# Optimization experiments

Measured on AMD Instinct MI355X. Metric: run time of the kernel, lower is better.

The kernel has to match this reference:

```python
import jax, jax.numpy as jnp
import numpy as np

EMBED_DIM = 512
NUM_HEADS = 8
HEAD_DIM = EMBED_DIM // NUM_HEADS
EDGE_DIM = 16
B, N = 2, 2048


def setup_inputs() -> dict:
    key = jax.random.key(0)
    ks = jax.random.split(key, 16)
    s = 1.0 / np.sqrt(EMBED_DIM)
    inp = {
        "x": jax.random.normal(ks[0], (B, N, EMBED_DIM), dtype=jnp.float32),
        "adjacency": jax.random.uniform(ks[1], (B, N, N), dtype=jnp.float32),
        # torch.nn.Linear stores weight as (out, in); we keep that convention
        "Wq": jax.random.uniform(ks[2], (EMBED_DIM, EMBED_DIM), minval=-s, maxval=s),
        "bq": jax.random.uniform(ks[3], (EMBED_DIM,), minval=-s, maxval=s),
        "Wk": jax.random.uniform(ks[4], (EMBED_DIM, EMBED_DIM), minval=-s, maxval=s),
        "bk": jax.random.uniform(ks[5], (EMBED_DIM,), minval=-s, maxval=s),
        "Wv": jax.random.uniform(ks[6], (EMBED_DIM, EMBED_DIM), minval=-s, maxval=s),
        "bv": jax.random.uniform(ks[7], (EMBED_DIM,), minval=-s, maxval=s),
        "Wo": jax.random.uniform(ks[8], (EMBED_DIM, EMBED_DIM), minval=-s, maxval=s),
        "bo": jax.random.uniform(ks[9], (EMBED_DIM,), minval=-s, maxval=s),
        # edge MLP: Linear(1 -> edge_dim) then Linear(edge_dim -> num_heads)
        "We1": jax.random.uniform(ks[10], (EDGE_DIM, 1), minval=-1.0, maxval=1.0),
        "be1": jax.random.uniform(ks[11], (EDGE_DIM,), minval=-1.0, maxval=1.0),
        "We2": jax.random.uniform(ks[12], (NUM_HEADS, EDGE_DIM), minval=-0.25, maxval=0.25),
        "be2": jax.random.uniform(ks[13], (NUM_HEADS,), minval=-0.25, maxval=0.25),
        "edge_bias": jnp.zeros((NUM_HEADS,), dtype=jnp.float32),
    }
    return inp


def reference(x, adjacency, Wq, bq, Wk, bk, Wv, bv, Wo, bo, We1, be1, We2, be2, edge_bias):
    b, n, _ = x.shape
    scale = HEAD_DIM ** (-0.5)

    def split_heads(t):  # (b, n, E) -> (b, H, n, d)
        return t.reshape(b, n, NUM_HEADS, HEAD_DIM).transpose(0, 2, 1, 3)

    q = split_heads(x @ Wq.T + bq)
    k = split_heads(x @ Wk.T + bk)
    v = split_heads(x @ Wv.T + bv)

    # (b, H, n, n)
    attn_scores = jnp.einsum('bhid,bhjd->bhij', q, k) * scale

    # edge MLP applied pointwise to each adjacency entry: 1 -> edge_dim -> num_heads
    # hidden: (b, n, n, edge_dim)
    hidden = jax.nn.relu(adjacency[..., None] * We1[:, 0] + be1)
    edge_attn = jnp.einsum('bijE,hE->bhij', hidden, We2) + be2[None, :, None, None]

    boost = adjacency[:, None, :, :] * edge_bias[None, :, None, None]
    attn_scores = attn_scores + edge_attn + boost

    attn_probs = jax.nn.softmax(attn_scores, axis=-1)
    out = jnp.einsum('bhij,bhjd->bhid', attn_probs, v)
    out = out.transpose(0, 2, 1, 3).reshape(b, n, EMBED_DIM)
    out = out @ Wo.T + bo
    return out
```

## Files before the change

kernel.cpp:

```cpp
#include <hip/hip_runtime.h>
#include <stdint.h>


#define SEQ 2048
#define EMB 512
#define NH  8
#define HD  64
#define NB  2
#define L2E 1.4426950408889634f

typedef unsigned int   u32;
typedef unsigned short u16;
typedef u32   u32x4  __attribute__((ext_vector_type(4)));
typedef float f32x4  __attribute__((ext_vector_type(4)));
typedef __bf16 bf16x8 __attribute__((ext_vector_type(8)));

#define MFMA16(a, b, c) __builtin_amdgcn_mfma_f32_16x16x32_bf16((a), (b), (c), 0, 0, 0)

static __device__ __forceinline__ u16 f2bf(float f) {
  return __builtin_bit_cast(u16, (__bf16)f);
}
static __device__ __forceinline__ bf16x8 ldfrag(const u16* p) {
  return __builtin_bit_cast(bf16x8, *(const u32x4*)p);
}

__global__ void prep_kernel(const float* __restrict__ x,
                            const float* __restrict__ Wq, const float* __restrict__ Wk,
                            const float* __restrict__ Wv, const float* __restrict__ Wo,
                            const float* __restrict__ We1, const float* __restrict__ be1,
                            const float* __restrict__ We2, const float* __restrict__ be2,
                            const float* __restrict__ ebias,
                            u16* __restrict__ xb, u16* __restrict__ wqkv,
                            u16* __restrict__ wob, float* __restrict__ co) {
  const int blk = blockIdx.x, tid = threadIdx.x;
  if (blk < 2048) {
    int i = (blk * 256 + tid) * 4;
    float4 v = *(const float4*)(x + i);
    u32 lo = (u32)f2bf(v.x) | ((u32)f2bf(v.y) << 16);
    u32 hi = (u32)f2bf(v.z) | ((u32)f2bf(v.w) << 16);
    *(uint2*)(xb + i) = make_uint2(lo, hi);
  } else if (blk < 3072) {
    int i = ((blk - 2048) * 256 + tid) * 4;
    int m = i >> 18;
    int off = i & 262143;
    const float* src = (m == 0) ? Wq : ((m == 1) ? Wk : ((m == 2) ? Wv : Wo));
    u16* dst = (m < 3) ? (wqkv + (size_t)m * 262144) : wob;
    float4 v = *(const float4*)(src + off);
    u32 lo = (u32)f2bf(v.x) | ((u32)f2bf(v.y) << 16);
    u32 hi = (u32)f2bf(v.z) | ((u32)f2bf(v.w) << 16);
    *(uint2*)(dst + off) = make_uint2(lo, hi);
  } else {
    const int e = tid & 15, h = tid >> 4;
    if (tid < 128) {
      co[49 + e * 8 + h] = 0.0f;
      if (h == 0) { co[17 + e] = 0.0f; co[33 + e] = 0.0f; }
    }
    __syncthreads();
    if (tid < 128) {
      float w1 = We1[e], b1 = be1[e], w2 = We2[h * 16 + e];
      float u0 = b1, u1 = w1 + b1;
      bool on  = (u0 >= 0.0f) && (u1 >= 0.0f);
      bool off = (u0 <= 0.0f) && (u1 <= 0.0f);
      bool crossing = (!on) && (!off);
      float ca = on ? (w2 * b1) : (crossing ? 0.5f * w2 * b1 : 0.0f);
      float cb = on ? (w2 * w1) : (crossing ? 0.5f * w2 * w1 : 0.0f);
      #pragma unroll
      for (int d = 1; d < 16; d <<= 1) { ca += __shfl_xor(ca, d); cb += __shfl_xor(cb, d); }
      if (e == 0) { co[h] = (be2[h] + ca) * L2E; co[8 + h] = (ebias[h] + cb) * L2E; }
      unsigned long long msk = __ballot(crossing);
      int midx = __popcll(msk & 0xFFFFull & ((1ull << e) - 1ull));
      int mcnt = __popcll(msk & 0xFFFFull);
      if (crossing) {
        co[49 + midx * 8 + h] = 0.5f * w2 * L2E;
        if (h == 0) { co[17 + midx] = w1; co[33 + midx] = b1; }
      }
      if (tid == 0) ((int*)co)[16] = mcnt;
    }
  }
}

#define LDA 40
__global__ __launch_bounds__(256) void gemm_qkv_kernel(
    const u16* __restrict__ A, const u16* __restrict__ Bm,
    const float* __restrict__ bq, const float* __restrict__ bk, const float* __restrict__ bv,
    u16* __restrict__ qh, u16* __restrict__ kh, u16* __restrict__ vh)
{
  __shared__ u16 As[64 * LDA];
  __shared__ u16 Bs[128 * LDA];
  const int tid = threadIdx.x;
  const int lane = tid & 63, w = tid >> 6;
  const int q = lane >> 4, l15 = lane & 15;
  const int m0 = blockIdx.y * 64;
  const int n0 = blockIdx.x * 128;

  f32x4 acc[4][2];
  f32x4 zero = {0.f, 0.f, 0.f, 0.f};
  #pragma unroll
  for (int i = 0; i < 4; i++) { acc[i][0] = zero; acc[i][1] = zero; }

  const bool isA = tid < 128;
  const int arow = tid >> 1, ahalf = tid & 1;
  const int brow = tid - 128;
  const u16* ga = A  + (size_t)(m0 + arow) * EMB + ahalf * 16;
  const u16* gb = Bm + (size_t)(n0 + brow) * EMB;
  u16* la = &As[arow * LDA + ahalf * 16];
  u16* lb = &Bs[brow * LDA];

  u32x4 p0, p1, p2, p3;
  if (isA) {
    p0 = *(const u32x4*)(ga); p1 = *(const u32x4*)(ga + 8); ga += 32;
  } else {
    p0 = *(const u32x4*)(gb);      p1 = *(const u32x4*)(gb + 8);
    p2 = *(const u32x4*)(gb + 16); p3 = *(const u32x4*)(gb + 24); gb += 32;
  }

  for (int k0 = 0; k0 < EMB; k0 += 32) {
    __syncthreads();
    if (isA) { *(u32x4*)(la) = p0; *(u32x4*)(la + 8) = p1; }
    else {
      *(u32x4*)(lb)      = p0; *(u32x4*)(lb + 8)  = p1;
      *(u32x4*)(lb + 16) = p2; *(u32x4*)(lb + 24) = p3;
    }
    __syncthreads();
    if (k0 + 32 < EMB) {
      if (isA) { p0 = *(const u32x4*)(ga); p1 = *(const u32x4*)(ga + 8); ga += 32; }
      else {
        p0 = *(const u32x4*)(gb);      p1 = *(const u32x4*)(gb + 8);
        p2 = *(const u32x4*)(gb + 16); p3 = *(const u32x4*)(gb + 24); gb += 32;
      }
    }
    bf16x8 af[4], bfr[2];
    #pragma unroll
    for (int mi = 0; mi < 4; mi++)
      af[mi] = ldfrag(&As[(mi*16 + l15) * LDA + q*8]);
    #pragma unroll
    for (int ni = 0; ni < 2; ni++)
      bfr[ni] = ldfrag(&Bs[(w*32 + ni*16 + l15) * LDA + q*8]);
    #pragma unroll
    for (int mi = 0; mi < 4; mi++)
      #pragma unroll
      for (int ni = 0; ni < 2; ni++)
        acc[mi][ni] = MFMA16(af[mi], bfr[ni], acc[mi][ni]);
  }

  const int mat = n0 >> 9;
  const float* bias = (mat == 0) ? bq : ((mat == 1) ? bk : bv);
  u16* dst = (mat == 0) ? qh : ((mat == 1) ? kh : vh);
  const float mul = (mat == 0) ? 0.125f * L2E : 1.0f;

  #pragma unroll
  for (int mi = 0; mi < 4; mi++) {
    int rowb = m0 + mi*16 + q*4;
    #pragma unroll
    for (int ni = 0; ni < 2; ni++) {
      int col = n0 + w*32 + ni*16 + l15;
      int oo = col & 511;
      float bsv = bias[oo];
      int hh = oo >> 6, dd = oo & 63;
      #pragma unroll
      for (int r = 0; r < 4; r++) {
        int grow = rowb + r;
        int b_ = grow >> 11, n_ = grow & 2047;
        float val = (acc[mi][ni][r] + bsv) * mul;
        dst[((size_t)(b_ * NH + hh) * SEQ + n_) * HD + dd] = f2bf(val);
      }
    }
  }
}

__global__ __launch_bounds__(256) void gemm_out_kernel(
    const u16* __restrict__ A, const u16* __restrict__ Bm,
    const float* __restrict__ bo, float* __restrict__ out)
{
  __shared__ u16 As[64 * LDA];
  __shared__ u16 Bs[128 * LDA];
  const int tid = threadIdx.x;
  const int lane = tid & 63, w = tid >> 6;
  const int q = lane >> 4, l15 = lane & 15;
  const int m0 = blockIdx.y * 64;
  const int n0 = blockIdx.x * 128;

  f32x4 acc[4][2];
  f32x4 zero = {0.f, 0.f, 0.f, 0.f};
  #pragma unroll
  for (int i = 0; i < 4; i++) { acc[i][0] = zero; acc[i][1] = zero; }

  const bool isA = tid < 128;
  const int arow = tid >> 1, ahalf = tid & 1;
  const int brow = tid - 128;
  const u16* ga = A  + (size_t)(m0 + arow) * EMB + ahalf * 16;
  const u16* gb = Bm + (size_t)(n0 + brow) * EMB;
  u16* la = &As[arow * LDA + ahalf * 16];
  u16* lb = &Bs[brow * LDA];

  u32x4 p0, p1, p2, p3;
  if (isA) {
    p0 = *(const u32x4*)(ga); p1 = *(const u32x4*)(ga + 8); ga += 32;
  } else {
    p0 = *(const u32x4*)(gb);      p1 = *(const u32x4*)(gb + 8);
    p2 = *(const u32x4*)(gb + 16); p3 = *(const u32x4*)(gb + 24); gb += 32;
  }

  for (int k0 = 0; k0 < EMB; k0 += 32) {
    __syncthreads();
    if (isA) { *(u32x4*)(la) = p0; *(u32x4*)(la + 8) = p1; }
    else {
      *(u32x4*)(lb)      = p0; *(u32x4*)(lb + 8)  = p1;
      *(u32x4*)(lb + 16) = p2; *(u32x4*)(lb + 24) = p3;
    }
    __syncthreads();
    if (k0 + 32 < EMB) {
      if (isA) { p0 = *(const u32x4*)(ga); p1 = *(const u32x4*)(ga + 8); ga += 32; }
      else {
        p0 = *(const u32x4*)(gb);      p1 = *(const u32x4*)(gb + 8);
        p2 = *(const u32x4*)(gb + 16); p3 = *(const u32x4*)(gb + 24); gb += 32;
      }
    }
    bf16x8 af[4], bfr[2];
    #pragma unroll
    for (int mi = 0; mi < 4; mi++)
      af[mi] = ldfrag(&As[(mi*16 + l15) * LDA + q*8]);
    #pragma unroll
    for (int ni = 0; ni < 2; ni++)
      bfr[ni] = ldfrag(&Bs[(w*32 + ni*16 + l15) * LDA + q*8]);
    #pragma unroll
    for (int mi = 0; mi < 4; mi++)
      #pragma unroll
      for (int ni = 0; ni < 2; ni++)
        acc[mi][ni] = MFMA16(af[mi], bfr[ni], acc[mi][ni]);
  }

  #pragma unroll
  for (int mi = 0; mi < 4; mi++) {
    int rowb = m0 + mi*16 + q*4;
    #pragma unroll
    for (int ni = 0; ni < 2; ni++) {
      int col = n0 + w*32 + ni*16 + l15;
      float bsv = bo[col];
      #pragma unroll
      for (int r = 0; r < 4; r++)
        out[(size_t)(rowb + r) * EMB + col] = acc[mi][ni][r] + bsv;
    }
  }
}

__global__ __launch_bounds__(256) void vtrans_kernel(const u16* __restrict__ vh, u16* __restrict__ vt) {
  __shared__ u16 Ts[64 * 72];
  const int b = blockIdx.z, h = blockIdx.y, j0 = blockIdx.x * 64;
  const int t = threadIdx.x;
  const u16* src = vh + ((size_t)(b * NH + h) * SEQ + j0) * HD;
  {
    int r = t >> 2, c = t & 3;
    *(u32x4*)&Ts[r*72 + c*16]     = *(const u32x4*)(src + r*HD + c*16);
    *(u32x4*)&Ts[r*72 + c*16 + 8] = *(const u32x4*)(src + r*HD + c*16 + 8);
  }
  __syncthreads();
  int d = t >> 2, jc = t & 3;
  u32 wv[8];
  #pragma unroll
  for (int p = 0; p < 8; p++) {
    u32 lo = Ts[(jc*16 + 2*p    ) * 72 + d];
    u32 hi = Ts[(jc*16 + 2*p + 1) * 72 + d];
    wv[p] = lo | (hi << 16);
  }
  u16* dst = vt + ((size_t)(b * NH + h) * HD + d) * SEQ + j0 + jc * 16;
  u32x4 w0 = {wv[0], wv[1], wv[2], wv[3]};
  u32x4 w1 = {wv[4], wv[5], wv[6], wv[7]};
  *(u32x4*)(dst)     = w0;
  *(u32x4*)(dst + 8) = w1;
}

template<int MT>
__device__ __forceinline__ void flash_body(
    u16* __restrict__ smem,
    const u16* __restrict__ qh, const u16* __restrict__ kh, const u16* __restrict__ vt,
    const float* __restrict__ adj, const float* __restrict__ coeff, u16* __restrict__ om)
{
  u16* Ks = smem;
  u16* Vs = smem + 9216;
  u16* Ps = smem + 18432;

  const int tid = threadIdx.x, lane = tid & 63, w = tid >> 6;
  const int q = lane >> 4, l15 = lane & 15;
  const int i0 = blockIdx.x * 64;
  const int h = blockIdx.y, b = blockIdx.z;
  const int bh = b * NH + h;
  const int jhalf = w >> 2, wrow = (w & 3) * 16;
  const int jbase = jhalf * 1024;

  const float Ah = coeff[h], Bh = coeff[8 + h];
  float ctr[MT > 0 ? MT : 1], dtr[MT > 0 ? MT : 1], wtr[MT > 0 ? MT : 1];
  #pragma unroll
  for (int t = 0; t < MT; t++) {
    ctr[t] = coeff[17 + t];
    dtr[t] = coeff[33 + t];
    wtr[t] = coeff[49 + t * 8 + h];
  }

  const u16* qbase = qh + ((size_t)bh * SEQ + i0 + wrow + l15) * HD + q * 8;
  bf16x8 qf0 = ldfrag(qbase);
  bf16x8 qf1 = ldfrag(qbase + 32);

  f32x4 O[4];
  f32x4 zero = {0.f, 0.f, 0.f, 0.f};
  #pragma unroll
  for (int dt = 0; dt < 4; dt++) O[dt] = zero;
  float lsum[4] = {0.f, 0.f, 0.f, 0.f};

  const float* abase = adj + ((size_t)b * SEQ + i0 + wrow + q * 4) * SEQ + jbase;

  const int shalf = tid >> 8, t8 = tid & 255;
  const int sr = t8 >> 2, sc = t8 & 3;
  const u16* kgs = kh + (size_t)bh * SEQ * HD + ((size_t)(shalf * 1024) + sr) * HD + sc * 16;
  const u16* vgs = vt + (size_t)bh * HD * SEQ + (size_t)sr * SEQ + shalf * 1024 + sc * 16;
  u16* kls = &Ks[(shalf * 64 + sr) * 72 + sc * 16];
  u16* vls = &Vs[(shalf * 64 + sr) * 72 + sc * 16];

  u16* psw = &Ps[w * 16 * 72];

  u32x4 pk0 = *(const u32x4*)(kgs);
  u32x4 pk1 = *(const u32x4*)(kgs + 8);
  u32x4 pv0 = *(const u32x4*)(vgs);
  u32x4 pv1 = *(const u32x4*)(vgs + 8);
  float padj[16];
  #pragma unroll
  for (int jt = 0; jt < 4; jt++)
    #pragma unroll
    for (int r = 0; r < 4; r++)
      padj[jt * 4 + r] = abase[(size_t)r * SEQ + jt * 16 + l15];

  for (int it = 0; it < 16; it++) {
    __syncthreads();
    *(u32x4*)(kls)     = pk0;
    *(u32x4*)(kls + 8) = pk1;
    *(u32x4*)(vls)     = pv0;
    *(u32x4*)(vls + 8) = pv1;
    __syncthreads();

    const int nxo = ((it + 1) & 15) * 64;
    pk0 = *(const u32x4*)(kgs + (size_t)nxo * HD);
    pk1 = *(const u32x4*)(kgs + (size_t)nxo * HD + 8);
    pv0 = *(const u32x4*)(vgs + nxo);
    pv1 = *(const u32x4*)(vgs + nxo + 8);

    f32x4 S[4];
    #pragma unroll
    for (int jt = 0; jt < 4; jt++) {
      bf16x8 kf0 = ldfrag(&Ks[(jhalf * 64 + jt * 16 + l15) * 72 + q * 8]);
      bf16x8 kf1 = ldfrag(&Ks[(jhalf * 64 + jt * 16 + l15) * 72 + 32 + q * 8]);
      f32x4 s = zero;
      s = MFMA16(qf0, kf0, s);
      s = MFMA16(qf1, kf1, s);
      S[jt] = s;
    }

    float eb[16];
    #pragma unroll
    for (int u = 0; u < 16; u++)
      eb[u] = fmaf(padj[u], Bh, Ah);
    #pragma unroll
    for (int t = 0; t < MT; t++)
      #pragma unroll
      for (int u = 0; u < 16; u++)
        eb[u] = fmaf(fabsf(fmaf(padj[u], ctr[t], dtr[t])), wtr[t], eb[u]);

    #pragma unroll
    for (int jt = 0; jt < 4; jt++)
      #pragma unroll
      for (int r = 0; r < 4; r++)
        padj[jt * 4 + r] = abase[(size_t)r * SEQ + nxo + jt * 16 + l15];

    #pragma unroll
    for (int jt = 0; jt < 4; jt++) {
      #pragma unroll
      for (int r = 0; r < 4; r++) {
        float p = __builtin_amdgcn_exp2f(S[jt][r] + eb[jt * 4 + r]);
        lsum[r] += p;
        psw[(q * 4 + r) * 72 + jt * 16 + l15] = f2bf(p);
      }
    }

    bf16x8 pf0 = ldfrag(&psw[l15 * 72 + q * 8]);
    bf16x8 pf1 = ldfrag(&psw[l15 * 72 + 32 + q * 8]);
    #pragma unroll
    for (int dt = 0; dt < 4; dt++) {
      bf16x8 vf0 = ldfrag(&Vs[(jhalf * 64 + dt * 16 + l15) * 72 + q * 8]);
      bf16x8 vf1 = ldfrag(&Vs[(jhalf * 64 + dt * 16 + l15) * 72 + 32 + q * 8]);
      O[dt] = MFMA16(pf0, vf0, O[dt]);
      O[dt] = MFMA16(pf1, vf1, O[dt]);
    }
  }

  #pragma unroll
  for (int r = 0; r < 4; r++) {
    float v = lsum[r];
    v += __shfl_xor(v, 1);
    v += __shfl_xor(v, 2);
    v += __shfl_xor(v, 4);
    v += __shfl_xor(v, 8);
    lsum[r] = v;
  }

  __syncthreads();
  f32x4* Of = (f32x4*)smem;
  f32x4* Lf = (f32x4*)((float*)smem + 5120);
  if (w >= 4) {
    const int bi = ((w & 3) * 64 + lane);
    #pragma unroll
    for (int dt = 0; dt < 4; dt++) Of[bi * 5 + dt] = O[dt];
    f32x4 lv = {lsum[0], lsum[1], lsum[2], lsum[3]};
    Lf[bi] = lv;
  }
  __syncthreads();
  if (w < 4) {
    const int bi = (w * 64 + lane);
    f32x4 lv = Lf[bi];
    float rl[4];
    #pragma unroll
    for (int r = 0; r < 4; r++) rl[r] = 1.0f / (lsum[r] + lv[r]);
    #pragma unroll
    for (int dt = 0; dt < 4; dt++) {
      f32x4 ov = Of[bi * 5 + dt];
      #pragma unroll
      for (int r = 0; r < 4; r++) {
        float val = (O[dt][r] + ov[r]) * rl[r];
        om[((size_t)b * SEQ + i0 + wrow + q * 4 + r) * EMB + h * HD + dt * 16 + l15] = f2bf(val);
      }
    }
  }
}

__global__ __launch_bounds__(512) void flash_kernel(
    const u16* __restrict__ qh, const u16* __restrict__ kh, const u16* __restrict__ vt,
    const float* __restrict__ adj, const float* __restrict__ coeff, u16* __restrict__ om)
{
  __shared__ __align__(16) u16 smem[27648];
  const int mt = ((const int*)coeff)[16];
  if (mt <= 4)      flash_body<4>(smem, qh, kh, vt, adj, coeff, om);
  else if (mt <= 8) flash_body<8>(smem, qh, kh, vt, adj, coeff, om);
  else              flash_body<16>(smem, qh, kh, vt, adj, coeff, om);
}

extern "C" void kernel_launch(void* const* d_in, const int* in_sizes, int n_in,
                              void* d_out, int out_size, void* d_ws, size_t ws_size,
                              hipStream_t stream) {
  const float* x     = (const float*)d_in[0];
  const float* adj   = (const float*)d_in[1];
  const float* Wq    = (const float*)d_in[2];
  const float* bq    = (const float*)d_in[3];
  const float* Wk    = (const float*)d_in[4];
  const float* bk    = (const float*)d_in[5];
  const float* Wv    = (const float*)d_in[6];
  const float* bv    = (const float*)d_in[7];
  const float* Wo    = (const float*)d_in[8];
  const float* bo    = (const float*)d_in[9];
  const float* We1   = (const float*)d_in[10];
  const float* be1   = (const float*)d_in[11];
  const float* We2   = (const float*)d_in[12];
  const float* be2   = (const float*)d_in[13];
  const float* ebias = (const float*)d_in[14];
  float* out = (float*)d_out;

  char* ws = (char*)d_ws;
  u16*   xb   = (u16*)(ws + 0);
  u16*   wqkv = (u16*)(ws + 4194304);
  u16*   wob  = (u16*)(ws + 5767168);
  u16*   qh   = (u16*)(ws + 6291456);
  u16*   kh   = (u16*)(ws + 10485760);
  u16*   vh   = (u16*)(ws + 14680064);
  u16*   vt   = (u16*)(ws + 18874368);
  u16*   om   = (u16*)(ws + 23068672);
  float* co   = (float*)(ws + 27262976);
  if (ws_size < 27264000) return;

  prep_kernel<<<3073, 256, 0, stream>>>(x, Wq, Wk, Wv, Wo, We1, be1, We2, be2, ebias,
                                        xb, wqkv, wob, co);
  gemm_qkv_kernel<<<dim3(12, 64), 256, 0, stream>>>(xb, wqkv, bq, bk, bv, qh, kh, vh);
  vtrans_kernel<<<dim3(32, NH, NB), 256, 0, stream>>>(vh, vt);
  flash_kernel<<<dim3(32, NH, NB), 512, 0, stream>>>(qh, kh, vt, adj, co, om);
  gemm_out_kernel<<<dim3(4, 64), 256, 0, stream>>>(om, wob, bo, out);
}
```

Baseline: 198.5 us.

## Write K/V in MFMA-fragment-swizzled layout and drop LDS staging in flash attention

The QKV GEMM epilogue now writes K and V directly in a swizzled layout that matches the MFMA fragment order, so the separate V-transpose kernel is removed. The flash kernel loads K/V fragments straight from global memory instead of staging them through shared memory with barriers. It also swaps MFMA operand order so each lane owns a single query row, which simplifies the row-sum reduction and vectorizes P and output stores. Adjacency is loaded as float4, and the output GEMM uses smaller 64x64 tiles to launch more blocks. The risk is that K/V tiles are read redundantly from global memory or L2 by each wave instead of being shared via LDS.

After: 208.2 us. 4.9% more time.

```diff
diff --git a/kernel.cpp b/kernel.cpp
--- a/kernel.cpp
+++ b/kernel.cpp
@@ -20,9 +20,13 @@
 static __device__ __forceinline__ u16 f2bf(float f) {
   return __builtin_bit_cast(u16, (__bf16)f);
 }
+static __device__ __forceinline__ u32 pack2(float a, float b) {
+  return (u32)f2bf(a) | ((u32)f2bf(b) << 16);
+}
 static __device__ __forceinline__ bf16x8 ldfrag(const u16* p) {
   return __builtin_bit_cast(bf16x8, *(const u32x4*)p);
 }
+
 
 __global__ void prep_kernel(const float* __restrict__ x,
                             const float* __restrict__ Wq, const float* __restrict__ Wk,
@@ -36,9 +40,7 @@
   if (blk < 2048) {
     int i = (blk * 256 + tid) * 4;
     float4 v = *(const float4*)(x + i);
-    u32 lo = (u32)f2bf(v.x) | ((u32)f2bf(v.y) << 16);
-    u32 hi = (u32)f2bf(v.z) | ((u32)f2bf(v.w) << 16);
-    *(uint2*)(xb + i) = make_uint2(lo, hi);
+    *(uint2*)(xb + i) = make_uint2(pack2(v.x, v.y), pack2(v.z, v.w));
   } else if (blk < 3072) {
     int i = ((blk - 2048) * 256 + tid) * 4;
     int m = i >> 18;
@@ -46,9 +48,7 @@
     const float* src = (m == 0) ? Wq : ((m == 1) ? Wk : ((m == 2) ? Wv : Wo));
     u16* dst = (m < 3) ? (wqkv + (size_t)m * 262144) : wob;
     float4 v = *(const float4*)(src + off);
-    u32 lo = (u32)f2bf(v.x) | ((u32)f2bf(v.y) << 16);
-    u32 hi = (u32)f2bf(v.z) | ((u32)f2bf(v.w) << 16);
-    *(uint2*)(dst + off) = make_uint2(lo, hi);
+    *(uint2*)(dst + off) = make_uint2(pack2(v.x, v.y), pack2(v.z, v.w));
   } else {
     const int e = tid & 15, h = tid >> 4;
     if (tid < 128) {
@@ -83,7 +83,7 @@
 __global__ __launch_bounds__(256) void gemm_qkv_kernel(
     const u16* __restrict__ A, const u16* __restrict__ Bm,
     const float* __restrict__ bq, const float* __restrict__ bk, const float* __restrict__ bv,
-    u16* __restrict__ qh, u16* __restrict__ kh, u16* __restrict__ vh)
+    u16* __restrict__ qh, u16* __restrict__ ksw, u16* __restrict__ vsw)
 {
   __shared__ u16 As[64 * LDA];
   __shared__ u16 Bs[128 * LDA];
@@ -144,9 +144,6 @@
   }
 
   const int mat = n0 >> 9;
-  const float* bias = (mat == 0) ? bq : ((mat == 1) ? bk : bv);
-  u16* dst = (mat == 0) ? qh : ((mat == 1) ? kh : vh);
-  const float mul = (mat == 0) ? 0.125f * L2E : 1.0f;
 
   #pragma unroll
   for (int mi = 0; mi < 4; mi++) {
@@ -155,14 +152,40 @@
     for (int ni = 0; ni < 2; ni++) {
       int col = n0 + w*32 + ni*16 + l15;
       int oo = col & 511;
-      float bsv = bias[oo];
       int hh = oo >> 6, dd = oo & 63;
-      #pragma unroll
-      for (int r = 0; r < 4; r++) {
-        int grow = rowb + r;
-        int b_ = grow >> 11, n_ = grow & 2047;
-        float val = (acc[mi][ni][r] + bsv) * mul;
-        dst[((size_t)(b_ * NH + hh) * SEQ + n_) * HD + dd] = f2bf(val);
+      if (mat == 0) {
+        float bsv = bq[oo];
+        #pragma unroll
+        for (int r = 0; r < 4; r++) {
+          int grow = rowb + r;
+          int b_ = grow >> 11, n_ = grow & 2047;
+          float val = (acc[mi][ni][r] + bsv) * (0.125f * L2E);
+          qh[((size_t)(b_ * NH + hh) * SEQ + n_) * HD + dd] = f2bf(val);
+        }
+      } else if (mat == 1) {
+        float bsv = bk[oo];
+        #pragma unroll
+        for (int r = 0; r < 4; r++) {
+          int grow = rowb + r;
+          int b_ = grow >> 11, n_ = grow & 2047;
+          float val = acc[mi][ni][r] + bsv;
+          size_t addr = (size_t)(b_ * NH + hh) * 131072
+                      + (n_ >> 4) * 1024 + ((dd >> 5) << 9)
+                      + ((((dd >> 3) & 3) * 16 + (n_ & 15)) << 3) + (dd & 7);
+          ksw[addr] = f2bf(val);
+        }
+      } else {
+        float bsv = bv[oo];
+        #pragma unroll
+        for (int r = 0; r < 4; r++) {
+          int grow = rowb + r;
+          int b_ = grow >> 11, n_ = grow & 2047;
+          float val = acc[mi][ni][r] + bsv;
+          size_t addr = (size_t)(b_ * NH + hh) * 131072
+                      + (n_ >> 6) * 4096 + ((dd >> 4) << 10) + (((n_ >> 5) & 1) << 9)
+                      + ((((n_ >> 3) & 3) * 16 + (dd & 15)) << 3) + (n_ & 7);
+          vsw[addr] = f2bf(val);
+        }
       }
     }
   }
@@ -173,123 +196,73 @@
     const float* __restrict__ bo, float* __restrict__ out)
 {
   __shared__ u16 As[64 * LDA];
-  __shared__ u16 Bs[128 * LDA];
+  __shared__ u16 Bs[64 * LDA];
   const int tid = threadIdx.x;
   const int lane = tid & 63, w = tid >> 6;
   const int q = lane >> 4, l15 = lane & 15;
   const int m0 = blockIdx.y * 64;
-  const int n0 = blockIdx.x * 128;
-
-  f32x4 acc[4][2];
+  const int n0 = blockIdx.x * 64;
+
+  f32x4 acc[4];
   f32x4 zero = {0.f, 0.f, 0.f, 0.f};
   #pragma unroll
-  for (int i = 0; i < 4; i++) { acc[i][0] = zero; acc[i][1] = zero; }
+  for (int i = 0; i < 4; i++) acc[i] = zero;
 
   const bool isA = tid < 128;
-  const int arow = tid >> 1, ahalf = tid & 1;
-  const int brow = tid - 128;
-  const u16* ga = A  + (size_t)(m0 + arow) * EMB + ahalf * 16;
-  const u16* gb = Bm + (size_t)(n0 + brow) * EMB;
-  u16* la = &As[arow * LDA + ahalf * 16];
-  u16* lb = &Bs[brow * LDA];
-
-  u32x4 p0, p1, p2, p3;
-  if (isA) {
-    p0 = *(const u32x4*)(ga); p1 = *(const u32x4*)(ga + 8); ga += 32;
-  } else {
-    p0 = *(const u32x4*)(gb);      p1 = *(const u32x4*)(gb + 8);
-    p2 = *(const u32x4*)(gb + 16); p3 = *(const u32x4*)(gb + 24); gb += 32;
-  }
+  const int row = isA ? (tid >> 1) : ((tid - 128) >> 1);
+  const int half = tid & 1;
+  const u16* g = (isA ? A + (size_t)(m0 + row) * EMB : Bm + (size_t)(n0 + row) * EMB)
+               + half * 16;
+  u16* l = (isA ? &As[row * LDA] : &Bs[row * LDA]) + half * 16;
+
+  u32x4 p0 = *(const u32x4*)(g);
+  u32x4 p1 = *(const u32x4*)(g + 8);
+  g += 32;
 
   for (int k0 = 0; k0 < EMB; k0 += 32) {
     __syncthreads();
-    if (isA) { *(u32x4*)(la) = p0; *(u32x4*)(la + 8) = p1; }
-    else {
-      *(u32x4*)(lb)      = p0; *(u32x4*)(lb + 8)  = p1;
-      *(u32x4*)(lb + 16) = p2; *(u32x4*)(lb + 24) = p3;
-    }
+    *(u32x4*)(l) = p0; *(u32x4*)(l + 8) = p1;
     __syncthreads();
     if (k0 + 32 < EMB) {
-      if (isA) { p0 = *(const u32x4*)(ga); p1 = *(const u32x4*)(ga + 8); ga += 32; }
-      else {
-        p0 = *(const u32x4*)(gb);      p1 = *(const u32x4*)(gb + 8);
-        p2 = *(const u32x4*)(gb + 16); p3 = *(const u32x4*)(gb + 24); gb += 32;
-      }
-    }
-    bf16x8 af[4], bfr[2];
+      p0 = *(const u32x4*)(g); p1 = *(const u32x4*)(g + 8); g += 32;
+    }
+    bf16x8 af[4], bfr;
     #pragma unroll
     for (int mi = 0; mi < 4; mi++)
       af[mi] = ldfrag(&As[(mi*16 + l15) * LDA + q*8]);
-    #pragma unroll
-    for (int ni = 0; ni < 2; ni++)
-      bfr[ni] = ldfrag(&Bs[(w*32 + ni*16 + l15) * LDA + q*8]);
+    bfr = ldfrag(&Bs[(w*16 + l15) * LDA + q*8]);
     #pragma unroll
     for (int mi = 0; mi < 4; mi++)
-      #pragma unroll
-      for (int ni = 0; ni < 2; ni++)
-        acc[mi][ni] = MFMA16(af[mi], bfr[ni], acc[mi][ni]);
-  }
-
+      acc[mi] = MFMA16(af[mi], bfr, acc[mi]);
+  }
+
+  int col = n0 + w*16 + l15;
+  float bsv = bo[col];
   #pragma unroll
   for (int mi = 0; mi < 4; mi++) {
     int rowb = m0 + mi*16 + q*4;
     #pragma unroll
-    for (int ni = 0; ni < 2; ni++) {
-      int col = n0 + w*32 + ni*16 + l15;
-      float bsv = bo[col];
-      #pragma unroll
-      for (int r = 0; r < 4; r++)
-        out[(size_t)(rowb + r) * EMB + col] = acc[mi][ni][r] + bsv;
-    }
-  }
-}
-
-__global__ __launch_bounds__(256) void vtrans_kernel(const u16* __restrict__ vh, u16* __restrict__ vt) {
-  __shared__ u16 Ts[64 * 72];
-  const int b = blockIdx.z, h = blockIdx.y, j0 = blockIdx.x * 64;
-  const int t = threadIdx.x;
-  const u16* src = vh + ((size_t)(b * NH + h) * SEQ + j0) * HD;
-  {
-    int r = t >> 2, c = t & 3;
-    *(u32x4*)&Ts[r*72 + c*16]     = *(const u32x4*)(src + r*HD + c*16);
-    *(u32x4*)&Ts[r*72 + c*16 + 8] = *(const u32x4*)(src + r*HD + c*16 + 8);
-  }
-  __syncthreads();
-  int d = t >> 2, jc = t & 3;
-  u32 wv[8];
-  #pragma unroll
-  for (int p = 0; p < 8; p++) {
-    u32 lo = Ts[(jc*16 + 2*p    ) * 72 + d];
-    u32 hi = Ts[(jc*16 + 2*p + 1) * 72 + d];
-    wv[p] = lo | (hi << 16);
-  }
-  u16* dst = vt + ((size_t)(b * NH + h) * HD + d) * SEQ + j0 + jc * 16;
-  u32x4 w0 = {wv[0], wv[1], wv[2], wv[3]};
-  u32x4 w1 = {wv[4], wv[5], wv[6], wv[7]};
-  *(u32x4*)(dst)     = w0;
-  *(u32x4*)(dst + 8) = w1;
+    for (int r = 0; r < 4; r++)
+      out[(size_t)(rowb + r) * EMB + col] = acc[mi][r] + bsv;
+  }
 }
 
 template<int MT>
 __device__ __forceinline__ void flash_body(
     u16* __restrict__ smem,
-    const u16* __restrict__ qh, const u16* __restrict__ kh, const u16* __restrict__ vt,
+    const u16* __restrict__ qh, const u16* __restrict__ ksw, const u16* __restrict__ vsw,
     const float* __restrict__ adj, const float* __restrict__ coeff, u16* __restrict__ om)
 {
-  u16* Ks = smem;
-  u16* Vs = smem + 9216;
-  u16* Ps = smem + 18432;
-
   const int tid = threadIdx.x, lane = tid & 63, w = tid >> 6;
   const int q = lane >> 4, l15 = lane & 15;
   const int i0 = blockIdx.x * 64;
   const int h = blockIdx.y, b = blockIdx.z;
   const int bh = b * NH + h;
-  const int jhalf = w >> 2, wrow = (w & 3) * 16;
-  const int jbase = jhalf * 1024;
+  const int iw = i0 + (w & 3) * 16;
+  const int jbase = (w >> 2) * 1024;
 
   const float Ah = coeff[h], Bh = coeff[8 + h];
-  float ctr[MT > 0 ? MT : 1], dtr[MT > 0 ? MT : 1], wtr[MT > 0 ? MT : 1];
+  float ctr[MT], dtr[MT], wtr[MT];
   #pragma unroll
   for (int t = 0; t < MT; t++) {
     ctr[t] = coeff[17 + t];
@@ -297,148 +270,114 @@
     wtr[t] = coeff[49 + t * 8 + h];
   }
 
-  const u16* qbase = qh + ((size_t)bh * SEQ + i0 + wrow + l15) * HD + q * 8;
-  bf16x8 qf0 = ldfrag(qbase);
-  bf16x8 qf1 = ldfrag(qbase + 32);
+  const u16* qrow = qh + ((size_t)bh * SEQ + iw + l15) * HD;
+  bf16x8 qf0 = ldfrag(qrow + q * 8);
+  bf16x8 qf1 = ldfrag(qrow + 32 + q * 8);
+
+  const u16* kbase = ksw + (size_t)bh * 131072 + jbase * 64 + lane * 8;
+  const u16* vbase = vsw + (size_t)bh * 131072 + jbase * 64 + lane * 8;
+  const float* arow = adj + ((size_t)b * SEQ + iw + l15) * SEQ + jbase + q * 4;
 
   f32x4 O[4];
   f32x4 zero = {0.f, 0.f, 0.f, 0.f};
   #pragma unroll
   for (int dt = 0; dt < 4; dt++) O[dt] = zero;
-  float lsum[4] = {0.f, 0.f, 0.f, 0.f};
-
-  const float* abase = adj + ((size_t)b * SEQ + i0 + wrow + q * 4) * SEQ + jbase;
-
-  const int shalf = tid >> 8, t8 = tid & 255;
-  const int sr = t8 >> 2, sc = t8 & 3;
-  const u16* kgs = kh + (size_t)bh * SEQ * HD + ((size_t)(shalf * 1024) + sr) * HD + sc * 16;
-  const u16* vgs = vt + (size_t)bh * HD * SEQ + (size_t)sr * SEQ + shalf * 1024 + sc * 16;
-  u16* kls = &Ks[(shalf * 64 + sr) * 72 + sc * 16];
-  u16* vls = &Vs[(shalf * 64 + sr) * 72 + sc * 16];
-
-  u16* psw = &Ps[w * 16 * 72];
-
-  u32x4 pk0 = *(const u32x4*)(kgs);
-  u32x4 pk1 = *(const u32x4*)(kgs + 8);
-  u32x4 pv0 = *(const u32x4*)(vgs);
-  u32x4 pv1 = *(const u32x4*)(vgs + 8);
-  float padj[16];
-  #pragma unroll
-  for (int jt = 0; jt < 4; jt++)
-    #pragma unroll
-    for (int r = 0; r < 4; r++)
-      padj[jt * 4 + r] = abase[(size_t)r * SEQ + jt * 16 + l15];
+  float lsum = 0.0f;
+
+  u16* psw = smem + w * 16 * 72;
 
   for (int it = 0; it < 16; it++) {
-    __syncthreads();
-    *(u32x4*)(kls)     = pk0;
-    *(u32x4*)(kls + 8) = pk1;
-    *(u32x4*)(vls)     = pv0;
-    *(u32x4*)(vls + 8) = pv1;
-    __syncthreads();
-
-    const int nxo = ((it + 1) & 15) * 64;
-    pk0 = *(const u32x4*)(kgs + (size_t)nxo * HD);
-    pk1 = *(const u32x4*)(kgs + (size_t)nxo * HD + 8);
-    pv0 = *(const u32x4*)(vgs + nxo);
-    pv1 = *(const u32x4*)(vgs + nxo + 8);
+    const int off = it * 4096;
+
+    bf16x8 kf[8];
+    #pragma unroll
+    for (int jt = 0; jt < 4; jt++) {
+      kf[jt*2]   = ldfrag(kbase + off + jt * 1024);
+      kf[jt*2+1] = ldfrag(kbase + off + jt * 1024 + 512);
+    }
+    float4 av[4];
+    #pragma unroll
+    for (int jt = 0; jt < 4; jt++)
+      av[jt] = *(const float4*)(arow + it * 64 + jt * 16);
 
     f32x4 S[4];
     #pragma unroll
     for (int jt = 0; jt < 4; jt++) {
-      bf16x8 kf0 = ldfrag(&Ks[(jhalf * 64 + jt * 16 + l15) * 72 + q * 8]);
-      bf16x8 kf1 = ldfrag(&Ks[(jhalf * 64 + jt * 16 + l15) * 72 + 32 + q * 8]);
-      f32x4 s = zero;
-      s = MFMA16(qf0, kf0, s);
-      s = MFMA16(qf1, kf1, s);
-      S[jt] = s;
-    }
-
-    float eb[16];
-    #pragma unroll
-    for (int u = 0; u < 16; u++)
-      eb[u] = fmaf(padj[u], Bh, Ah);
-    #pragma unroll
-    for (int t = 0; t < MT; t++)
-      #pragma unroll
-      for (int u = 0; u < 16; u++)
-        eb[u] = fmaf(fabsf(fmaf(padj[u], ctr[t], dtr[t])), wtr[t], eb[u]);
-
-    #pragma unroll
-    for (int jt = 0; jt < 4; jt++)
-      #pragma unroll
-      for (int r = 0; r < 4; r++)
-        padj[jt * 4 + r] = abase[(size_t)r * SEQ + nxo + jt * 16 + l15];
+      f32x4 s = MFMA16(kf[jt*2], qf0, zero);
+      S[jt] = MFMA16(kf[jt*2+1], qf1, s);
+    }
+
+    bf16x8 vf[8];
+    #pragma unroll
+    for (int dt = 0; dt < 4; dt++) {
+      vf[dt*2]   = ldfrag(vbase + off + dt * 1024);
+      vf[dt*2+1] = ldfrag(vbase + off + dt * 1024 + 512);
+    }
 
     #pragma unroll
     for (int jt = 0; jt < 4; jt++) {
+      float p[4];
       #pragma unroll
       for (int r = 0; r < 4; r++) {
-        float p = __builtin_amdgcn_exp2f(S[jt][r] + eb[jt * 4 + r]);
-        lsum[r] += p;
-        psw[(q * 4 + r) * 72 + jt * 16 + l15] = f2bf(p);
+        float a = ((const float*)&av[jt])[r];
+        float e = fmaf(a, Bh, Ah);
+        #pragma unroll
+        for (int t = 0; t < MT; t++)
+          e = fmaf(fabsf(fmaf(a, ctr[t], dtr[t])), wtr[t], e);
+        p[r] = __builtin_amdgcn_exp2f(S[jt][r] + e);
+        lsum += p[r];
       }
-    }
-
-    bf16x8 pf0 = ldfrag(&psw[l15 * 72 + q * 8]);
-    bf16x8 pf1 = ldfrag(&psw[l15 * 72 + 32 + q * 8]);
+      *(uint2*)(psw + l15 * 72 + jt * 16 + q * 4) =
+          make_uint2(pack2(p[0], p[1]), pack2(p[2], p[3]));
+    }
+
+    bf16x8 pf0 = ldfrag(psw + l15 * 72 + q * 8);
+    bf16x8 pf1 = ldfrag(psw + l15 * 72 + 32 + q * 8);
     #pragma unroll
     for (int dt = 0; dt < 4; dt++) {
-      bf16x8 vf0 = ldfrag(&Vs[(jhalf * 64 + dt * 16 + l15) * 72 + q * 8]);
-      bf16x8 vf1 = ldfrag(&Vs[(jhalf * 64 + dt * 16 + l15) * 72 + 32 + q * 8]);
-      O[dt] = MFMA16(pf0, vf0, O[dt]);
-      O[dt] = MFMA16(pf1, vf1, O[dt]);
-    }
-  }
-
-  #pragma unroll
-  for (int r = 0; r < 4; r++) {
-    float v = lsum[r];
-    v += __shfl_xor(v, 1);
-    v += __shfl_xor(v, 2);
-    v += __shfl_xor(v, 4);
-    v += __shfl_xor(v, 8);
-    lsum[r] = v;
-  }
+      O[dt] = MFMA16(vf[dt*2],   pf0, O[dt]);
+      O[dt] = MFMA16(vf[dt*2+1], pf1, O[dt]);
+    }
+  }
+
+  lsum += __shfl_xor(lsum, 16);
+  lsum += __shfl_xor(lsum, 32);
 
   __syncthreads();
-  f32x4* Of = (f32x4*)smem;
-  f32x4* Lf = (f32x4*)((float*)smem + 5120);
+  float* fbuf = (float*)smem;
   if (w >= 4) {
-    const int bi = ((w & 3) * 64 + lane);
-    #pragma unroll
-    for (int dt = 0; dt < 4; dt++) Of[bi * 5 + dt] = O[dt];
-    f32x4 lv = {lsum[0], lsum[1], lsum[2], lsum[3]};
-    Lf[bi] = lv;
+    int bi = ((w & 3) * 64 + lane) * 17;
+    #pragma unroll
+    for (int dt = 0; dt < 4; dt++)
+      #pragma unroll
+      for (int r = 0; r < 4; r++) fbuf[bi + dt * 4 + r] = O[dt][r];
+    fbuf[bi + 16] = lsum;
   }
   __syncthreads();
   if (w < 4) {
-    const int bi = (w * 64 + lane);
-    f32x4 lv = Lf[bi];
-    float rl[4];
-    #pragma unroll
-    for (int r = 0; r < 4; r++) rl[r] = 1.0f / (lsum[r] + lv[r]);
+    int bi = (w * 64 + lane) * 17;
+    float rl = 1.0f / (lsum + fbuf[bi + 16]);
+    u16* orow = om + ((size_t)b * SEQ + iw + l15) * EMB + h * HD + q * 4;
     #pragma unroll
     for (int dt = 0; dt < 4; dt++) {
-      f32x4 ov = Of[bi * 5 + dt];
-      #pragma unroll
-      for (int r = 0; r < 4; r++) {
-        float val = (O[dt][r] + ov[r]) * rl[r];
-        om[((size_t)b * SEQ + i0 + wrow + q * 4 + r) * EMB + h * HD + dt * 16 + l15] = f2bf(val);
-      }
-    }
-  }
-}
-
-__global__ __launch_bounds__(512) void flash_kernel(
-    const u16* __restrict__ qh, const u16* __restrict__ kh, const u16* __restrict__ vt,
+      float v0 = (O[dt][0] + fbuf[bi + dt * 4 + 0]) * rl;
+      float v1 = (O[dt][1] + fbuf[bi + dt * 4 + 1]) * rl;
+      float v2 = (O[dt][2] + fbuf[bi + dt * 4 + 2]) * rl;
+      float v3 = (O[dt][3] + fbuf[bi + dt * 4 + 3]) * rl;
+      *(uint2*)(orow + dt * 16) = make_uint2(pack2(v0, v1), pack2(v2, v3));
+    }
+  }
+}
+
+__global__ __launch_bounds__(512, 4) void flash_kernel(
+    const u16* __restrict__ qh, const u16* __restrict__ ksw, const u16* __restrict__ vsw,
     const float* __restrict__ adj, const float* __restrict__ coeff, u16* __restrict__ om)
 {
-  __shared__ __align__(16) u16 smem[27648];
+  __shared__ __align__(16) u16 smem[8 * 16 * 72];
   const int mt = ((const int*)coeff)[16];
-  if (mt <= 4)      flash_body<4>(smem, qh, kh, vt, adj, coeff, om);
-  else if (mt <= 8) flash_body<8>(smem, qh, kh, vt, adj, coeff, om);
-  else              flash_body<16>(smem, qh, kh, vt, adj, coeff, om);
+  if (mt <= 4)      flash_body<4>(smem, qh, ksw, vsw, adj, coeff, om);
+  else if (mt <= 8) flash_body<8>(smem, qh, ksw, vsw, adj, coeff, om);
+  else              flash_body<16>(smem, qh, ksw, vsw, adj, coeff, om);
 }
 
 extern "C" void kernel_launch(void* const* d_in, const int* in_sizes, int n_in,
@@ -466,17 +405,15 @@
   u16*   wqkv = (u16*)(ws + 4194304);
   u16*   wob  = (u16*)(ws + 5767168);
   u16*   qh   = (u16*)(ws + 6291456);
-  u16*   kh   = (u16*)(ws + 10485760);
-  u16*   vh   = (u16*)(ws + 14680064);
-  u16*   vt   = (u16*)(ws + 18874368);
-  u16*   om   = (u16*)(ws + 23068672);
-  float* co   = (float*)(ws + 27262976);
-  if (ws_size < 27264000) return;
+  u16*   ksw  = (u16*)(ws + 10485760);
+  u16*   vsw  = (u16*)(ws + 14680064);
+  u16*   om   = (u16*)(ws + 18874368);
+  float* co   = (float*)(ws + 23068672);
+  if (ws_size < 23069696) return;
 
   prep_kernel<<<3073, 256, 0, stream>>>(x, Wq, Wk, Wv, Wo, We1, be1, We2, be2, ebias,
                                         xb, wqkv, wob, co);
-  gemm_qkv_kernel<<<dim3(12, 64), 256, 0, stream>>>(xb, wqkv, bq, bk, bv, qh, kh, vh);
-  vtrans_kernel<<<dim3(32, NH, NB), 256, 0, stream>>>(vh, vt);
-  flash_kernel<<<dim3(32, NH, NB), 512, 0, stream>>>(qh, kh, vt, adj, co, om);
-  gemm_out_kernel<<<dim3(4, 64), 256, 0, stream>>>(om, wob, bo, out);
-}
+  gemm_qkv_kernel<<<dim3(12, 64), 256, 0, stream>>>(xb, wqkv, bq, bk, bv, qh, ksw, vsw);
+  flash_kernel<<<dim3(32, NH, NB), 512, 0, stream>>>(qh, ksw, vsw, adj, co, om);
+  gemm_out_kernel<<<dim3(8, 64), 256, 0, stream>>>(om, wob, bo, out);
+}
```
